# Optimization experiments

Hardware: AMD Instinct MI355X
Metric: run time of the kernel (lower is better)

Reference implementation:

```python
import jax, jax.numpy as jnp
import numpy as np

N_EMBED = 1024
N_HEAD = 16
SEQ = 2048
BATCH = 2


def setup_inputs() -> dict:
    key = jax.random.key(0)
    ks = jax.random.split(key, 5)
    scale_in = 1.0 / np.sqrt(N_EMBED)
    x = jax.random.normal(ks[0], (BATCH, SEQ, N_EMBED), dtype=jnp.float32)
    # attn_proj: Linear(n_embed, 3*n_embed); stored as [in, out] so y = x @ W + b
    W_qkv = jax.random.normal(ks[1], (N_EMBED, 3 * N_EMBED), dtype=jnp.float32) * scale_in
    b_qkv = jax.random.normal(ks[2], (3 * N_EMBED,), dtype=jnp.float32) * 0.01
    # fin_proj: Linear(n_embed, n_embed)
    W_out = jax.random.normal(ks[3], (N_EMBED, N_EMBED), dtype=jnp.float32) * scale_in
    b_out = jax.random.normal(ks[4], (N_EMBED,), dtype=jnp.float32) * 0.01
    return {"x": x, "W_qkv": W_qkv, "b_qkv": b_qkv, "W_out": W_out, "b_out": b_out}


def reference(x, W_qkv, b_qkv, W_out, b_out):
    B, S, D = x.shape
    H = N_HEAD
    hd = D // H
    qkv = x @ W_qkv + b_qkv  # [B, S, 3D]
    q, k, v = jnp.split(qkv, 3, axis=-1)
    # [B, H, S, hd]
    q = q.reshape(B, S, H, hd).transpose(0, 2, 1, 3)
    k = k.reshape(B, S, H, hd).transpose(0, 2, 1, 3)
    v = v.reshape(B, S, H, hd).transpose(0, 2, 1, 3)
    scores = jnp.einsum("bhqd,bhkd->bhqk", q, k) * (1.0 / np.sqrt(hd))
    causal = jnp.tril(jnp.ones((S, S), dtype=bool))  # lower-triangular mask
    scores = jnp.where(causal[None, None], scores, -jnp.inf)
    probs = jax.nn.softmax(scores, axis=-1)
    # dropout is identity in eval mode (inference reference)
    attn = jnp.einsum("bhqk,bhkd->bhqd", probs, v)  # [B, H, S, hd]
    attn = attn.transpose(0, 2, 1, 3).reshape(B, S, D)
    return attn @ W_out + b_out
```

## Files before the change

### kernel.cpp

```cpp
#include <hip/hip_runtime.h>

typedef short bf16x8 __attribute__((ext_vector_type(8)));
typedef short bf16x4 __attribute__((ext_vector_type(4)));
typedef float f32x4 __attribute__((ext_vector_type(4)));
typedef int i32x4 __attribute__((ext_vector_type(4)));
typedef int i32x2 __attribute__((ext_vector_type(2)));

#define MFMA16x16x32(a, b, c) __builtin_amdgcn_mfma_f32_16x16x32_bf16(a, b, c, 0, 0, 0)
#define TRR(dst, a) asm volatile("ds_read_b64_tr_b16 %0, %1" : "=v"(dst) : "v"(a))

__device__ __forceinline__ unsigned short f2bf(float f) {
  union { float f; unsigned u; } v; v.f = f;
  unsigned u = v.u + 0x7FFFu + ((v.u >> 16) & 1u);
  return (unsigned short)(u >> 16);
}

__device__ __forceinline__ unsigned cvtpk(float lo, float hi) {
  unsigned r;
  asm("v_cvt_pk_bf16_f32 %0, %1, %2" : "=v"(r) : "v"(lo), "v"(hi));
  return r;
}

__device__ __forceinline__ float max3f(float a, float b, float c) {
  float d;
  asm("v_max3_f32 %0, %1, %2, %3" : "=v"(d) : "v"(a), "v"(b), "v"(c));
  return d;
}

__device__ __forceinline__ void gload16(const void* g, void* l) {
  __builtin_amdgcn_global_load_lds((const __attribute__((address_space(1))) void*)g,
                                   (__attribute__((address_space(3))) void*)l, 16, 0, 0);
}

__device__ __forceinline__ unsigned ldsoff(const void* p) {
  return (unsigned)(unsigned long long)(const __attribute__((address_space(3))) void*)p;
}

__global__ __launch_bounds__(256) void prep(const float* __restrict__ x,
                                            unsigned short* __restrict__ xb,
                                            const float* __restrict__ Wq,
                                            unsigned short* __restrict__ WqT,
                                            const float* __restrict__ Wo,
                                            unsigned short* __restrict__ WoT) {
  __shared__ float tile[32][33];
  int bid = blockIdx.x;
  int t = threadIdx.x;
  if (bid < 2048) {
    long i = (long)bid * 256 + t;
    const float4* p = reinterpret_cast<const float4*>(x + i * 8);
    float4 a = p[0], b = p[1];
    i32x4 o;
    o[0] = cvtpk(a.x, a.y); o[1] = cvtpk(a.z, a.w);
    o[2] = cvtpk(b.x, b.y); o[3] = cvtpk(b.z, b.w);
    *reinterpret_cast<i32x4*>(xb + i * 8) = o;
    return;
  }
  const float* W; unsigned short* Wt; int N, bx, by;
  if (bid < 5120) {
    W = Wq; Wt = WqT; N = 3072;
    int r = bid - 2048; bx = r % 96; by = r / 96;
  } else {
    W = Wo; Wt = WoT; N = 1024;
    int r = bid - 5120; bx = r & 31; by = r >> 5;
  }
  const int K = 1024;
  int tx = t & 31, ty = t >> 5;
  int n0 = bx << 5, k0 = by << 5;
#pragma unroll
  for (int i = 0; i < 32; i += 8)
    tile[ty + i][tx] = W[(long)(k0 + ty + i) * N + n0 + tx];
  __syncthreads();
#pragma unroll
  for (int i = 0; i < 32; i += 8)
    Wt[(long)(n0 + ty + i) * K + k0 + tx] = f2bf(tile[tx][ty + i]);
}

template <int BF16OUT>
__global__ __launch_bounds__(256) void gemm_bt(const unsigned short* __restrict__ A,
                                               const unsigned short* __restrict__ Bt,
                                               const float* __restrict__ bias,
                                               void* __restrict__ Cv,
                                               int M, int N, int K) {
  __shared__ __align__(128) unsigned short As[3][4096];
  __shared__ __align__(128) unsigned short Bs[3][4096];
  int t = threadIdx.x;
  int w = t >> 6, l = t & 63;
  int g = l >> 4, m16 = l & 15;
  int wr = w >> 1, wc = w & 1;
  int nwg = gridDim.x * gridDim.y;
  int f = blockIdx.y * gridDim.x + blockIdx.x;
  int q8 = nwg >> 3;
  int s = (f & 7) * q8 + (f >> 3);
  int bx = s % gridDim.x, by = s / gridDim.x;
  long am0 = (long)by << 7;
  long bn0 = (long)bx << 7;

  int seg0 = w, seg1 = 4 + w;
  int fl0 = (seg0 << 9) + (l << 3), fl1 = (seg1 << 9) + (l << 3);
  int r0 = fl0 >> 5, c0 = fl0 & 31;
  int r1 = fl1 >> 5, c1 = fl1 & 31;

  f32x4 acc[4][4];
#pragma unroll
  for (int i = 0; i < 4; ++i)
#pragma unroll
    for (int j = 0; j < 4; ++j) acc[i][j] = (f32x4){0.f, 0.f, 0.f, 0.f};

  gload16(A + (am0 + r0) * K + c0, &As[0][seg0 << 9]);
  gload16(A + (am0 + r1) * K + c1, &As[0][seg1 << 9]);
  gload16(Bt + (bn0 + r0) * K + c0, &Bs[0][seg0 << 9]);
  gload16(Bt + (bn0 + r1) * K + c1, &Bs[0][seg1 << 9]);
  gload16(A + (am0 + r0) * K + 32 + c0, &As[1][seg0 << 9]);
  gload16(A + (am0 + r1) * K + 32 + c1, &As[1][seg1 << 9]);
  gload16(Bt + (bn0 + r0) * K + 32 + c0, &Bs[1][seg0 << 9]);
  gload16(Bt + (bn0 + r1) * K + 32 + c1, &Bs[1][seg1 << 9]);

  int cur = 0;
  for (int k0 = 0; k0 < K; k0 += 32) {
    if (k0 + 32 < K)
      asm volatile("s_waitcnt vmcnt(4)" ::: "memory");
    else
      asm volatile("s_waitcnt vmcnt(0)" ::: "memory");
    __syncthreads();
    if (k0 + 64 < K) {
      int kn = k0 + 64;
      int nb = cur + 2; if (nb >= 3) nb -= 3;
      gload16(A + (am0 + r0) * K + kn + c0, &As[nb][seg0 << 9]);
      gload16(A + (am0 + r1) * K + kn + c1, &As[nb][seg1 << 9]);
      gload16(Bt + (bn0 + r0) * K + kn + c0, &Bs[nb][seg0 << 9]);
      gload16(Bt + (bn0 + r1) * K + kn + c1, &Bs[nb][seg1 << 9]);
    }
    bf16x8 af[4], bfr[4];
#pragma unroll
    for (int im = 0; im < 4; ++im)
      af[im] = *(const bf16x8*)&As[cur][((wr << 6) + (im << 4) + m16) * 32 + (g << 3)];
#pragma unroll
    for (int in = 0; in < 4; ++in)
      bfr[in] = *(const bf16x8*)&Bs[cur][((wc << 6) + (in << 4) + m16) * 32 + (g << 3)];
    __builtin_amdgcn_s_setprio(1);
#pragma unroll
    for (int im = 0; im < 4; ++im)
#pragma unroll
      for (int in = 0; in < 4; ++in)
        acc[im][in] = MFMA16x16x32(af[im], bfr[in], acc[im][in]);
    __builtin_amdgcn_s_setprio(0);
    cur = cur == 2 ? 0 : cur + 1;
  }

#pragma unroll
  for (int im = 0; im < 4; ++im) {
#pragma unroll
    for (int in = 0; in < 4; ++in) {
      long col = bn0 + (wc << 6) + (in << 4) + m16;
      float bval = bias[col];
#pragma unroll
      for (int r = 0; r < 4; ++r) {
        long row = am0 + (wr << 6) + (im << 4) + (g << 2) + r;
        float v = acc[im][in][r] + bval;
        if (BF16OUT)
          ((unsigned short*)Cv)[row * N + col] = f2bf(v);
        else
          ((float*)Cv)[row * N + col] = v;
      }
    }
  }
}

__global__ __launch_bounds__(256, 3) void attn_fwd(const unsigned short* __restrict__ qkv,
                                                   unsigned short* __restrict__ out) {
  const int D3 = 3072;
  const float C1 = 0.18033688f;
  const float THR = 11.5415603f;
  __shared__ __align__(128) unsigned short Ks[2][4096];
  __shared__ __align__(128) unsigned short Vs[2][4096];
  int b = blockIdx.x >> 4, h = blockIdx.x & 15;
  int yy = blockIdx.y;
  int qt = (yy & 1) ? (31 - (yy >> 1)) : (yy >> 1);
  int t = threadIdx.x;
  int w = t >> 6, l = t & 63;
  int g = l >> 4, m16 = l & 15;
  long base = (long)b * 2048 * D3;
  const unsigned short* kbase = qkv + base + 1024 + h * 64;
  const unsigned short* vbase = qkv + base + 2048 + h * 64;

  int l8 = l >> 3, sc = l & 7;
  int kof = (w * 8 + l8) * D3 + ((sc ^ l8) << 3);
  int s0 = w * 8 + l8;
  int vof = ((s0 & 15) * 4 + (sc >> 1)) * D3 + ((s0 >> 4) << 4) + ((sc & 1) << 3);
  const f32x4 zero4 = (f32x4){0.f, 0.f, 0.f, 0.f};

  int qrow = (qt << 6) + (w << 4) + m16;
  const unsigned short* qp = qkv + base + (long)qrow * D3 + h * 64;
  bf16x8 qf0 = *(const bf16x8*)(qp + g * 8);
  bf16x8 qf1 = *(const bf16x8*)(qp + 32 + g * 8);

  f32x4 O[4];
#pragma unroll
  for (int d = 0; d < 4; ++d) O[d] = zero4;
  f32x4 lsv = zero4;
  float m2 = -1e30f;
  int nt = qt + 1;

  gload16(kbase + kof, &Ks[0][w << 9]);
  gload16(kbase + 32 * D3 + kof, &Ks[0][2048 + (w << 9)]);
  gload16(vbase + vof, &Vs[0][w << 9]);
  gload16(vbase + vof + 32, &Vs[0][2048 + (w << 9)]);

  int buf = 0;
  for (int ss = 0; ss < nt; ++ss) {
    asm volatile("s_waitcnt vmcnt(0)" ::: "memory");
    __syncthreads();
    if (ss + 1 < nt) {
      long off = (long)(ss + 1) * 64 * D3;
      gload16(kbase + off + kof, &Ks[buf ^ 1][w << 9]);
      gload16(kbase + off + 32 * D3 + kof, &Ks[buf ^ 1][2048 + (w << 9)]);
      gload16(vbase + off + vof, &Vs[buf ^ 1][w << 9]);
      gload16(vbase + off + vof + 32, &Vs[buf ^ 1][2048 + (w << 9)]);
    }

    unsigned va = ldsoff(&Vs[buf][0]) + (g << 7) + (m16 << 3);
    bf16x4 t0[4], t1[4], t2[4], t3[4];
#pragma unroll
    for (int d = 0; d < 4; ++d) {
      unsigned a = va + (d << 11);
      TRR(t0[d], a);
      TRR(t1[d], a + 512);
      TRR(t2[d], a + 1024);
      TRR(t3[d], a + 1536);
    }
    const char* kbuf = (const char*)&Ks[buf][0];
    int swz = m16 & 7;
    f32x4 st[4];
    __builtin_amdgcn_s_setprio(1);
#pragma unroll
    for (int T = 0; T < 4; ++T) {
      const char* rp = kbuf + (((T << 4) + m16) << 7);
      bf16x8 kf0 = *(const bf16x8*)(rp + ((g ^ swz) << 4));
      bf16x8 kf1 = *(const bf16x8*)(rp + (((4 + g) ^ swz) << 4));
      st[T] = MFMA16x16x32(kf0, qf0, zero4);
      st[T] = MFMA16x16x32(kf1, qf1, st[T]);
    }
    __builtin_amdgcn_s_setprio(0);

    if (ss == nt - 1) {
      int rq = qrow - (ss << 6);
#pragma unroll
      for (int T = 0; T < 4; ++T)
#pragma unroll
        for (int r = 0; r < 4; ++r)
          if ((T << 4) + (g << 2) + r > rq) st[T][r] = -3e38f;
    }
    float tm[4];
#pragma unroll
    for (int T = 0; T < 4; ++T)
      tm[T] = max3f(fmaxf(st[T][0], st[T][1]), st[T][2], st[T][3]);
    float tmax = fmaxf(max3f(tm[0], tm[1], tm[2]), tm[3]);
    tmax = fmaxf(tmax, __shfl_xor(tmax, 16));
    tmax = fmaxf(tmax, __shfl_xor(tmax, 32));
    float tsc2 = tmax * C1;
    bool skip = __all(tsc2 <= m2 + THR);
    float mnew2 = skip ? m2 : fmaxf(m2, tsc2);
    float p[4][4];
    f32x4 ts4 = zero4;
#pragma unroll
    for (int T = 0; T < 4; ++T)
#pragma unroll
      for (int r = 0; r < 4; ++r) {
        float e = __builtin_amdgcn_exp2f(fmaf(st[T][r], C1, -mnew2));
        p[T][r] = e;
        ts4[r] += e;
      }
    if (!skip) {
      float alpha = __builtin_amdgcn_exp2f(m2 - mnew2);
      lsv *= alpha;
#pragma unroll
      for (int d = 0; d < 4; ++d) O[d] *= alpha;
      m2 = mnew2;
    }
    lsv += ts4;

    i32x4 w0, w1;
    w0[0] = cvtpk(p[0][0], p[0][1]); w0[1] = cvtpk(p[0][2], p[0][3]);
    w0[2] = cvtpk(p[1][0], p[1][1]); w0[3] = cvtpk(p[1][2], p[1][3]);
    w1[0] = cvtpk(p[2][0], p[2][1]); w1[1] = cvtpk(p[2][2], p[2][3]);
    w1[2] = cvtpk(p[3][0], p[3][1]); w1[3] = cvtpk(p[3][2], p[3][3]);
    bf16x8 pb0 = __builtin_bit_cast(bf16x8, w0);
    bf16x8 pb1 = __builtin_bit_cast(bf16x8, w1);

    asm volatile("s_waitcnt lgkmcnt(0)" ::: "memory");
    __builtin_amdgcn_sched_barrier(0);

    bf16x8 vfA[4], vfB[4];
#pragma unroll
    for (int d = 0; d < 4; ++d) {
      vfA[d] = __builtin_shufflevector(t0[d], t1[d], 0, 1, 2, 3, 4, 5, 6, 7);
      vfB[d] = __builtin_shufflevector(t2[d], t3[d], 0, 1, 2, 3, 4, 5, 6, 7);
    }
    __builtin_amdgcn_s_setprio(1);
#pragma unroll
    for (int d = 0; d < 4; ++d) {
      O[d] = MFMA16x16x32(vfA[d], pb0, O[d]);
      O[d] = MFMA16x16x32(vfB[d], pb1, O[d]);
    }
    __builtin_amdgcn_s_setprio(0);
    buf ^= 1;
  }

  float s = (lsv[0] + lsv[1]) + (lsv[2] + lsv[3]);
  s += __shfl_xor(s, 16);
  s += __shfl_xor(s, 32);
  float inv = 1.0f / s;
  unsigned short* op = out + (long)(b * 2048 + qrow) * 1024 + h * 64;
#pragma unroll
  for (int d = 0; d < 4; ++d) {
    i32x2 pk;
    pk[0] = (int)cvtpk(O[d][0] * inv, O[d][1] * inv);
    pk[1] = (int)cvtpk(O[d][2] * inv, O[d][3] * inv);
    *reinterpret_cast<i32x2*>(op + (d << 4) + (g << 2)) = pk;
  }
}

extern "C" void kernel_launch(void* const* d_in, const int* in_sizes, int n_in,
                              void* d_out, int out_size, void* d_ws, size_t ws_size,
                              hipStream_t stream) {
  const float* x     = (const float*)d_in[0];
  const float* W_qkv = (const float*)d_in[1];
  const float* b_qkv = (const float*)d_in[2];
  const float* W_out = (const float*)d_in[3];
  const float* b_out = (const float*)d_in[4];

  char* ws = (char*)d_ws;
  unsigned short* xb    = (unsigned short*)ws;
  unsigned short* wqkvT = (unsigned short*)(ws + (8l << 20));
  unsigned short* woutT = (unsigned short*)(ws + (14l << 20));
  unsigned short* qkv   = (unsigned short*)(ws + (16l << 20));

  prep<<<6144, 256, 0, stream>>>(x, xb, W_qkv, wqkvT, W_out, woutT);
  gemm_bt<1><<<dim3(24, 32), 256, 0, stream>>>(xb, wqkvT, b_qkv, (void*)qkv, 4096, 3072, 1024);
  attn_fwd<<<dim3(32, 32), 256, 0, stream>>>(qkv, xb);
  gemm_bt<0><<<dim3(8, 32), 256, 0, stream>>>(xb, woutT, b_out, d_out, 4096, 1024, 1024);
}
```

Before: 110.4 us.

## Make attention kernel persistent with atomic work queue, longest tiles first

The attention kernel becomes persistent: 768 blocks repeatedly claim (batch, head, query-tile) work items from a global atomic counter, with the longest causal tiles handed out first. The counter is reset inside the prep kernel, and the workspace layout is shifted to make room for it. This targets load imbalance and tail idle time that come from uneven causal tile lengths under static grid scheduling. The cost is one atomic plus an extra block barrier per work item, and the code depends on the prep kernel having reset the counter.

```diff
diff --git a/kernel.cpp b/kernel.cpp
--- a/kernel.cpp
+++ b/kernel.cpp
@@ -41,10 +41,12 @@
                                             const float* __restrict__ Wq,
                                             unsigned short* __restrict__ WqT,
                                             const float* __restrict__ Wo,
-                                            unsigned short* __restrict__ WoT) {
+                                            unsigned short* __restrict__ WoT,
+                                            int* __restrict__ ctr) {
   __shared__ float tile[32][33];
   int bid = blockIdx.x;
   int t = threadIdx.x;
+  if (bid == 0 && t == 0) *ctr = 0;
   if (bid < 2048) {
     long i = (long)bid * 256 + t;
     const float4* p = reinterpret_cast<const float4*>(x + i * 8);
@@ -167,21 +169,17 @@
 }
 
 __global__ __launch_bounds__(256, 3) void attn_fwd(const unsigned short* __restrict__ qkv,
-                                                   unsigned short* __restrict__ out) {
+                                                   unsigned short* __restrict__ out,
+                                                   int* __restrict__ ctr) {
   const int D3 = 3072;
   const float C1 = 0.18033688f;
   const float THR = 11.5415603f;
   __shared__ __align__(128) unsigned short Ks[2][4096];
   __shared__ __align__(128) unsigned short Vs[2][4096];
-  int b = blockIdx.x >> 4, h = blockIdx.x & 15;
-  int yy = blockIdx.y;
-  int qt = (yy & 1) ? (31 - (yy >> 1)) : (yy >> 1);
+  __shared__ int s_idx;
   int t = threadIdx.x;
   int w = t >> 6, l = t & 63;
   int g = l >> 4, m16 = l & 15;
-  long base = (long)b * 2048 * D3;
-  const unsigned short* kbase = qkv + base + 1024 + h * 64;
-  const unsigned short* vbase = qkv + base + 2048 + h * 64;
 
   int l8 = l >> 3, sc = l & 7;
   int kof = (w * 8 + l8) * D3 + ((sc ^ l8) << 3);
@@ -189,134 +187,147 @@
   int vof = ((s0 & 15) * 4 + (sc >> 1)) * D3 + ((s0 >> 4) << 4) + ((sc & 1) << 3);
   const f32x4 zero4 = (f32x4){0.f, 0.f, 0.f, 0.f};
 
-  int qrow = (qt << 6) + (w << 4) + m16;
-  const unsigned short* qp = qkv + base + (long)qrow * D3 + h * 64;
-  bf16x8 qf0 = *(const bf16x8*)(qp + g * 8);
-  bf16x8 qf1 = *(const bf16x8*)(qp + 32 + g * 8);
-
-  f32x4 O[4];
-#pragma unroll
-  for (int d = 0; d < 4; ++d) O[d] = zero4;
-  f32x4 lsv = zero4;
-  float m2 = -1e30f;
-  int nt = qt + 1;
-
-  gload16(kbase + kof, &Ks[0][w << 9]);
-  gload16(kbase + 32 * D3 + kof, &Ks[0][2048 + (w << 9)]);
-  gload16(vbase + vof, &Vs[0][w << 9]);
-  gload16(vbase + vof + 32, &Vs[0][2048 + (w << 9)]);
-
-  int buf = 0;
-  for (int ss = 0; ss < nt; ++ss) {
-    asm volatile("s_waitcnt vmcnt(0)" ::: "memory");
+  for (;;) {
+    if (t == 0) s_idx = atomicAdd(ctr, 1);
     __syncthreads();
-    if (ss + 1 < nt) {
-      long off = (long)(ss + 1) * 64 * D3;
-      gload16(kbase + off + kof, &Ks[buf ^ 1][w << 9]);
-      gload16(kbase + off + 32 * D3 + kof, &Ks[buf ^ 1][2048 + (w << 9)]);
-      gload16(vbase + off + vof, &Vs[buf ^ 1][w << 9]);
-      gload16(vbase + off + vof + 32, &Vs[buf ^ 1][2048 + (w << 9)]);
+    int idx = s_idx;
+    if (idx >= 1024) return;
+    int qt = 31 - (idx >> 5);
+    int bh = idx & 31;
+    int b = bh >> 4, h = bh & 15;
+    long base = (long)b * 2048 * D3;
+    const unsigned short* kbase = qkv + base + 1024 + h * 64;
+    const unsigned short* vbase = qkv + base + 2048 + h * 64;
+
+    int qrow = (qt << 6) + (w << 4) + m16;
+    const unsigned short* qp = qkv + base + (long)qrow * D3 + h * 64;
+    bf16x8 qf0 = *(const bf16x8*)(qp + g * 8);
+    bf16x8 qf1 = *(const bf16x8*)(qp + 32 + g * 8);
+
+    f32x4 O[4];
+#pragma unroll
+    for (int d = 0; d < 4; ++d) O[d] = zero4;
+    f32x4 lsv = zero4;
+    float m2 = -1e30f;
+    int nt = qt + 1;
+
+    gload16(kbase + kof, &Ks[0][w << 9]);
+    gload16(kbase + 32 * D3 + kof, &Ks[0][2048 + (w << 9)]);
+    gload16(vbase + vof, &Vs[0][w << 9]);
+    gload16(vbase + vof + 32, &Vs[0][2048 + (w << 9)]);
+
+    int buf = 0;
+    for (int ss = 0; ss < nt; ++ss) {
+      asm volatile("s_waitcnt vmcnt(0)" ::: "memory");
+      __syncthreads();
+      if (ss + 1 < nt) {
+        long off = (long)(ss + 1) * 64 * D3;
+        gload16(kbase + off + kof, &Ks[buf ^ 1][w << 9]);
+        gload16(kbase + off + 32 * D3 + kof, &Ks[buf ^ 1][2048 + (w << 9)]);
+        gload16(vbase + off + vof, &Vs[buf ^ 1][w << 9]);
+        gload16(vbase + off + vof + 32, &Vs[buf ^ 1][2048 + (w << 9)]);
+      }
+
+      unsigned va = ldsoff(&Vs[buf][0]) + (g << 7) + (m16 << 3);
+      bf16x4 t0[4], t1[4], t2[4], t3[4];
+#pragma unroll
+      for (int d = 0; d < 4; ++d) {
+        unsigned a = va + (d << 11);
+        TRR(t0[d], a);
+        TRR(t1[d], a + 512);
+        TRR(t2[d], a + 1024);
+        TRR(t3[d], a + 1536);
+      }
+      const char* kbuf = (const char*)&Ks[buf][0];
+      int swz = m16 & 7;
+      f32x4 st[4];
+      __builtin_amdgcn_s_setprio(1);
+#pragma unroll
+      for (int T = 0; T < 4; ++T) {
+        const char* rp = kbuf + (((T << 4) + m16) << 7);
+        bf16x8 kf0 = *(const bf16x8*)(rp + ((g ^ swz) << 4));
+        bf16x8 kf1 = *(const bf16x8*)(rp + (((4 + g) ^ swz) << 4));
+        st[T] = MFMA16x16x32(kf0, qf0, zero4);
+        st[T] = MFMA16x16x32(kf1, qf1, st[T]);
+      }
+      __builtin_amdgcn_s_setprio(0);
+
+      if (ss == nt - 1) {
+        int rq = qrow - (ss << 6);
+#pragma unroll
+        for (int T = 0; T < 4; ++T)
+#pragma unroll
+          for (int r = 0; r < 4; ++r)
+            if ((T << 4) + (g << 2) + r > rq) st[T][r] = -3e38f;
+      }
+      float tm[4];
+#pragma unroll
+      for (int T = 0; T < 4; ++T)
+        tm[T] = max3f(fmaxf(st[T][0], st[T][1]), st[T][2], st[T][3]);
+      float tmax = fmaxf(max3f(tm[0], tm[1], tm[2]), tm[3]);
+      tmax = fmaxf(tmax, __shfl_xor(tmax, 16));
+      tmax = fmaxf(tmax, __shfl_xor(tmax, 32));
+      float tsc2 = tmax * C1;
+      bool skip = __all(tsc2 <= m2 + THR);
+      float mnew2 = skip ? m2 : fmaxf(m2, tsc2);
+      float p[4][4];
+      f32x4 ts4 = zero4;
+#pragma unroll
+      for (int T = 0; T < 4; ++T)
+#pragma unroll
+        for (int r = 0; r < 4; ++r) {
+          float e = __builtin_amdgcn_exp2f(fmaf(st[T][r], C1, -mnew2));
+          p[T][r] = e;
+          ts4[r] += e;
+        }
+      if (!skip) {
+        float alpha = __builtin_amdgcn_exp2f(m2 - mnew2);
+        lsv *= alpha;
+#pragma unroll
+        for (int d = 0; d < 4; ++d) O[d] *= alpha;
+        m2 = mnew2;
+      }
+      lsv += ts4;
+
+      i32x4 w0, w1;
+      w0[0] = cvtpk(p[0][0], p[0][1]); w0[1] = cvtpk(p[0][2], p[0][3]);
+      w0[2] = cvtpk(p[1][0], p[1][1]); w0[3] = cvtpk(p[1][2], p[1][3]);
+      w1[0] = cvtpk(p[2][0], p[2][1]); w1[1] = cvtpk(p[2][2], p[2][3]);
+      w1[2] = cvtpk(p[3][0], p[3][1]); w1[3] = cvtpk(p[3][2], p[3][3]);
+      bf16x8 pb0 = __builtin_bit_cast(bf16x8, w0);
+      bf16x8 pb1 = __builtin_bit_cast(bf16x8, w1);
+
+      asm volatile("s_waitcnt lgkmcnt(0)" ::: "memory");
+      __builtin_amdgcn_sched_barrier(0);
+
+      bf16x8 vfA[4], vfB[4];
+#pragma unroll
+      for (int d = 0; d < 4; ++d) {
+        vfA[d] = __builtin_shufflevector(t0[d], t1[d], 0, 1, 2, 3, 4, 5, 6, 7);
+        vfB[d] = __builtin_shufflevector(t2[d], t3[d], 0, 1, 2, 3, 4, 5, 6, 7);
+      }
+      __builtin_amdgcn_s_setprio(1);
+#pragma unroll
+      for (int d = 0; d < 4; ++d) {
+        O[d] = MFMA16x16x32(vfA[d], pb0, O[d]);
+        O[d] = MFMA16x16x32(vfB[d], pb1, O[d]);
+      }
+      __builtin_amdgcn_s_setprio(0);
+      buf ^= 1;
     }
 
-    unsigned va = ldsoff(&Vs[buf][0]) + (g << 7) + (m16 << 3);
-    bf16x4 t0[4], t1[4], t2[4], t3[4];
+    float s = (lsv[0] + lsv[1]) + (lsv[2] + lsv[3]);
+    s += __shfl_xor(s, 16);
+    s += __shfl_xor(s, 32);
+    float inv = 1.0f / s;
+    unsigned short* op = out + (long)(b * 2048 + qrow) * 1024 + h * 64;
 #pragma unroll
     for (int d = 0; d < 4; ++d) {
-      unsigned a = va + (d << 11);
-      TRR(t0[d], a);
-      TRR(t1[d], a + 512);
-      TRR(t2[d], a + 1024);
-      TRR(t3[d], a + 1536);
+      i32x2 pk;
+      pk[0] = (int)cvtpk(O[d][0] * inv, O[d][1] * inv);
+      pk[1] = (int)cvtpk(O[d][2] * inv, O[d][3] * inv);
+      *reinterpret_cast<i32x2*>(op + (d << 4) + (g << 2)) = pk;
     }
-    const char* kbuf = (const char*)&Ks[buf][0];
-    int swz = m16 & 7;
-    f32x4 st[4];
-    __builtin_amdgcn_s_setprio(1);
-#pragma unroll
-    for (int T = 0; T < 4; ++T) {
-      const char* rp = kbuf + (((T << 4) + m16) << 7);
-      bf16x8 kf0 = *(const bf16x8*)(rp + ((g ^ swz) << 4));
-      bf16x8 kf1 = *(const bf16x8*)(rp + (((4 + g) ^ swz) << 4));
-      st[T] = MFMA16x16x32(kf0, qf0, zero4);
-      st[T] = MFMA16x16x32(kf1, qf1, st[T]);
-    }
-    __builtin_amdgcn_s_setprio(0);
-
-    if (ss == nt - 1) {
-      int rq = qrow - (ss << 6);
-#pragma unroll
-      for (int T = 0; T < 4; ++T)
-#pragma unroll
-        for (int r = 0; r < 4; ++r)
-          if ((T << 4) + (g << 2) + r > rq) st[T][r] = -3e38f;
-    }
-    float tm[4];
-#pragma unroll
-    for (int T = 0; T < 4; ++T)
-      tm[T] = max3f(fmaxf(st[T][0], st[T][1]), st[T][2], st[T][3]);
-    float tmax = fmaxf(max3f(tm[0], tm[1], tm[2]), tm[3]);
-    tmax = fmaxf(tmax, __shfl_xor(tmax, 16));
-    tmax = fmaxf(tmax, __shfl_xor(tmax, 32));
-    float tsc2 = tmax * C1;
-    bool skip = __all(tsc2 <= m2 + THR);
-    float mnew2 = skip ? m2 : fmaxf(m2, tsc2);
-    float p[4][4];
-    f32x4 ts4 = zero4;
-#pragma unroll
-    for (int T = 0; T < 4; ++T)
-#pragma unroll
-      for (int r = 0; r < 4; ++r) {
-        float e = __builtin_amdgcn_exp2f(fmaf(st[T][r], C1, -mnew2));
-        p[T][r] = e;
-        ts4[r] += e;
-      }
-    if (!skip) {
-      float alpha = __builtin_amdgcn_exp2f(m2 - mnew2);
-      lsv *= alpha;
-#pragma unroll
-      for (int d = 0; d < 4; ++d) O[d] *= alpha;
-      m2 = mnew2;
-    }
-    lsv += ts4;
-
-    i32x4 w0, w1;
-    w0[0] = cvtpk(p[0][0], p[0][1]); w0[1] = cvtpk(p[0][2], p[0][3]);
-    w0[2] = cvtpk(p[1][0], p[1][1]); w0[3] = cvtpk(p[1][2], p[1][3]);
-    w1[0] = cvtpk(p[2][0], p[2][1]); w1[1] = cvtpk(p[2][2], p[2][3]);
-    w1[2] = cvtpk(p[3][0], p[3][1]); w1[3] = cvtpk(p[3][2], p[3][3]);
-    bf16x8 pb0 = __builtin_bit_cast(bf16x8, w0);
-    bf16x8 pb1 = __builtin_bit_cast(bf16x8, w1);
-
-    asm volatile("s_waitcnt lgkmcnt(0)" ::: "memory");
-    __builtin_amdgcn_sched_barrier(0);
-
-    bf16x8 vfA[4], vfB[4];
-#pragma unroll
-    for (int d = 0; d < 4; ++d) {
-      vfA[d] = __builtin_shufflevector(t0[d], t1[d], 0, 1, 2, 3, 4, 5, 6, 7);
-      vfB[d] = __builtin_shufflevector(t2[d], t3[d], 0, 1, 2, 3, 4, 5, 6, 7);
-    }
-    __builtin_amdgcn_s_setprio(1);
-#pragma unroll
-    for (int d = 0; d < 4; ++d) {
-      O[d] = MFMA16x16x32(vfA[d], pb0, O[d]);
-      O[d] = MFMA16x16x32(vfB[d], pb1, O[d]);
-    }
-    __builtin_amdgcn_s_setprio(0);
-    buf ^= 1;
-  }
-
-  float s = (lsv[0] + lsv[1]) + (lsv[2] + lsv[3]);
-  s += __shfl_xor(s, 16);
-  s += __shfl_xor(s, 32);
-  float inv = 1.0f / s;
-  unsigned short* op = out + (long)(b * 2048 + qrow) * 1024 + h * 64;
-#pragma unroll
-  for (int d = 0; d < 4; ++d) {
-    i32x2 pk;
-    pk[0] = (int)cvtpk(O[d][0] * inv, O[d][1] * inv);
-    pk[1] = (int)cvtpk(O[d][2] * inv, O[d][3] * inv);
-    *reinterpret_cast<i32x2*>(op + (d << 4) + (g << 2)) = pk;
   }
 }
 
@@ -330,13 +341,14 @@
   const float* b_out = (const float*)d_in[4];
 
   char* ws = (char*)d_ws;
-  unsigned short* xb    = (unsigned short*)ws;
-  unsigned short* wqkvT = (unsigned short*)(ws + (8l << 20));
-  unsigned short* woutT = (unsigned short*)(ws + (14l << 20));
-  unsigned short* qkv   = (unsigned short*)(ws + (16l << 20));
-
-  prep<<<6144, 256, 0, stream>>>(x, xb, W_qkv, wqkvT, W_out, woutT);
+  int* ctr = (int*)ws;
+  unsigned short* xb    = (unsigned short*)(ws + 256);
+  unsigned short* wqkvT = (unsigned short*)(ws + 256 + (8l << 20));
+  unsigned short* woutT = (unsigned short*)(ws + 256 + (14l << 20));
+  unsigned short* qkv   = (unsigned short*)(ws + 256 + (16l << 20));
+
+  prep<<<6144, 256, 0, stream>>>(x, xb, W_qkv, wqkvT, W_out, woutT, ctr);
   gemm_bt<1><<<dim3(24, 32), 256, 0, stream>>>(xb, wqkvT, b_qkv, (void*)qkv, 4096, 3072, 1024);
-  attn_fwd<<<dim3(32, 32), 256, 0, stream>>>(qkv, xb);
+  attn_fwd<<<768, 256, 0, stream>>>(qkv, xb, ctr);
   gemm_bt<0><<<dim3(8, 32), 256, 0, stream>>>(xb, woutT, b_out, d_out, 4096, 1024, 1024);
 }
```

New measurement: 116.9 us. 5.8% more time.
